# Kernel optimization log

Measured on AMD Instinct MI355X. Metric: run time of the kernel, lower is better.

Reference implementation:

```python
import jax, jax.numpy as jnp
import numpy as np

N_NODES = 100000
N_EDGES = 1600000
D_IN = 64
D_OUT = 64


def _sage_conv(x, Wl, b, Wr, src, dst, inv_deg):
    # mean-aggregate neighbor features: gather x[src], scatter-sum into dst, divide by degree
    agg = jax.ops.segment_sum(x[src], dst, num_segments=N_NODES)  # [N, d]
    agg = agg * inv_deg                                            # mean with deg clamped >= 1
    # PyG SAGEConv: lin_l(agg) (with bias) + lin_r(x) (no bias)
    return agg @ Wl.T + b + x @ Wr.T


def setup_inputs() -> dict:
    key = jax.random.key(0)
    ks = jax.random.split(key, 8)
    x = jax.random.normal(ks[0], (N_NODES, D_IN), dtype=jnp.float32)
    edge_index = jax.random.randint(ks[1], (2, N_EDGES), 0, N_NODES, dtype=jnp.int64)
    s1 = 1.0 / np.sqrt(D_IN)
    s2 = 1.0 / np.sqrt(D_OUT)
    Wl1 = jax.random.uniform(ks[2], (D_OUT, D_IN), jnp.float32, -s1, s1)
    b1 = jnp.zeros((D_OUT,), jnp.float32)
    Wr1 = jax.random.uniform(ks[3], (D_OUT, D_IN), jnp.float32, -s1, s1)
    Wl2 = jax.random.uniform(ks[4], (D_OUT, D_OUT), jnp.float32, -s2, s2)
    b2 = jnp.zeros((D_OUT,), jnp.float32)
    Wr2 = jax.random.uniform(ks[5], (D_OUT, D_OUT), jnp.float32, -s2, s2)
    return {"x": x, "edge_index": edge_index, "Wl1": Wl1, "b1": b1, "Wr1": Wr1,
            "Wl2": Wl2, "b2": b2, "Wr2": Wr2}


def reference(x, edge_index, Wl1, b1, Wr1, Wl2, b2, Wr2):
    src, dst = edge_index[0], edge_index[1]
    deg = jax.ops.segment_sum(jnp.ones((N_EDGES,), jnp.float32), dst, num_segments=N_NODES)
    inv_deg = (1.0 / jnp.maximum(deg, 1.0))[:, None]  # [N, 1]
    h = _sage_conv(x, Wl1, b1, Wr1, src, dst, inv_deg)
    h = _sage_conv(h, Wl2, b2, Wr2, src, dst, inv_deg)
    return h
```

## Files before the change

kernel.cpp:

```cpp
#include <hip/hip_runtime.h>
#include <hip/hip_bf16.h>

#define NN 100000
#define NE 1600000
#define NB 196
#define BCAP 9216
#define BIN_CHUNK 8192
#define BIN_BLKS ((NE + BIN_CHUNK - 1) / BIN_CHUNK)

typedef __attribute__((ext_vector_type(8))) short bf16x8;
typedef __attribute__((ext_vector_type(4))) float f32x4;

__device__ inline unsigned short f2bf(float f) {
    union { __hip_bfloat16 h; unsigned short u; } c;
    c.h = __float2bfloat16(f);
    return c.u;
}

__global__ __launch_bounds__(256) void k_prep(const float* __restrict__ x,
                                              unsigned short* __restrict__ xb,
                                              const float* __restrict__ Wl1,
                                              const float* __restrict__ Wr1,
                                              const float* __restrict__ Wl2,
                                              const float* __restrict__ Wr2,
                                              unsigned short* __restrict__ Wc1,
                                              unsigned short* __restrict__ Wc2,
                                              int* __restrict__ gcur) {
    int i = blockIdx.x * 256 + threadIdx.x;
    if (i < NB) gcur[i] = i * BCAP;
    if (i < 4096) {
        int fo = i >> 6, k = i & 63;
        Wc1[fo * 128 + k]      = f2bf(Wl1[i]);
        Wc1[fo * 128 + 64 + k] = f2bf(Wr1[i]);
        Wc2[fo * 128 + k]      = f2bf(Wl2[i]);
        Wc2[fo * 128 + 64 + k] = f2bf(Wr2[i]);
    }
    if (i < NN * 64 / 8) {
        const float4* p = (const float4*)(x + (size_t)i * 8);
        float4 v0 = p[0], v1 = p[1];
        union { bf16x8 v; unsigned short u[8]; } c;
        c.u[0] = f2bf(v0.x); c.u[1] = f2bf(v0.y); c.u[2] = f2bf(v0.z); c.u[3] = f2bf(v0.w);
        c.u[4] = f2bf(v1.x); c.u[5] = f2bf(v1.y); c.u[6] = f2bf(v1.z); c.u[7] = f2bf(v1.w);
        *(bf16x8*)(xb + (size_t)i * 8) = c.v;
    }
}

__global__ __launch_bounds__(256) void k_bin(const int* __restrict__ src,
                                             const int* __restrict__ dst,
                                             int* __restrict__ gcur,
                                             unsigned* __restrict__ binned) {
    __shared__ int hist[NB];
    __shared__ int base[NB];
    __shared__ int lcur[NB];
    const int t = threadIdx.x;
    const int e0 = blockIdx.x * BIN_CHUNK;
    const int n4 = min(BIN_CHUNK, NE - e0) >> 2;
    for (int i = t; i < NB; i += 256) { hist[i] = 0; lcur[i] = 0; }
    __syncthreads();
    const int4* d4p = (const int4*)(dst + e0);
    const int4* s4p = (const int4*)(src + e0);
    for (int i = t; i < n4; i += 256) {
        int4 d = d4p[i];
        atomicAdd(&hist[d.x >> 9], 1);
        atomicAdd(&hist[d.y >> 9], 1);
        atomicAdd(&hist[d.z >> 9], 1);
        atomicAdd(&hist[d.w >> 9], 1);
    }
    __syncthreads();
    for (int i = t; i < NB; i += 256) {
        int h = hist[i];
        base[i] = h ? atomicAdd(&gcur[i], h) : 0;
    }
    __syncthreads();
    for (int i = t; i < n4; i += 256) {
        int4 d = d4p[i];
        int4 s = s4p[i];
        #define PLACE(dd, ss) {                                         \
            int b = (dd) >> 9;                                          \
            int p = base[b] + atomicAdd(&lcur[b], 1);                   \
            binned[p] = ((unsigned)((dd) & 511) << 17) | (unsigned)(ss);}
        PLACE(d.x, s.x) PLACE(d.y, s.y) PLACE(d.z, s.z) PLACE(d.w, s.w)
        #undef PLACE
    }
}

__global__ __launch_bounds__(256) void k_csr(const int* __restrict__ gcur,
                                             unsigned* __restrict__ binned,
                                             int2* __restrict__ noff,
                                             float* __restrict__ inv) {
    __shared__ unsigned buf[BCAP];
    __shared__ int h[512];
    __shared__ int off[512];
    __shared__ int lcur[512];
    __shared__ int s[256];
    const int b = blockIdx.x;
    const int t = threadIdx.x;
    const int base = b * BCAP;
    const int cnt = min(gcur[b] - base, BCAP);
    for (int i = t; i < 512; i += 256) h[i] = 0;
    __syncthreads();
    for (int i = t; i < cnt; i += 256) {
        unsigned v = binned[base + i];
        buf[i] = v;
        atomicAdd(&h[v >> 17], 1);
    }
    __syncthreads();
    int a0 = h[2 * t], a1 = h[2 * t + 1];
    s[t] = a0 + a1;
    __syncthreads();
    #pragma unroll
    for (int o = 1; o < 256; o <<= 1) {
        int u = (t >= o) ? s[t - o] : 0;
        __syncthreads();
        s[t] += u;
        __syncthreads();
    }
    int ex = s[t] - (a0 + a1);
    off[2 * t] = ex;          lcur[2 * t] = ex;
    off[2 * t + 1] = ex + a0; lcur[2 * t + 1] = ex + a0;
    __syncthreads();
    for (int i = t; i < cnt; i += 256) {
        unsigned v = buf[i];
        int dl = v >> 17;
        int p = atomicAdd(&lcur[dl], 1);
        binned[base + p] = v & 0x1FFFFu;
    }
    #pragma unroll
    for (int q = 0; q < 2; ++q) {
        int l = 2 * t + q;
        int node = b * 512 + l;
        if (node < NN) {
            int st = base + off[l];
            noff[node] = make_int2(st, st + h[l]);
            inv[node] = 1.0f / fmaxf((float)h[l], 1.0f);
        }
    }
}

__global__ __launch_bounds__(512) void k_fused(const unsigned short* __restrict__ feat,
                                               const int2* __restrict__ noff,
                                               const unsigned* __restrict__ csr,
                                               const float* __restrict__ inv,
                                               const unsigned short* __restrict__ Wc,
                                               const float* __restrict__ bias,
                                               float* __restrict__ Cf,
                                               unsigned short* __restrict__ Cb) {
    __shared__ unsigned short sA[64 * 72];
    const int t = threadIdx.x;
    const int n0 = blockIdx.x * 64;

    {
        const int g = t >> 3;
        const int p = t & 7;
        const int node = n0 + g;
        float a[8] = {0.f, 0.f, 0.f, 0.f, 0.f, 0.f, 0.f, 0.f};
        float iv = 0.f;
        if (node < NN) {
            int2 oe = noff[node];
            int beg = oe.x, end = oe.y;
            iv = inv[node];

            #define UNPK(uu, k)                                        \
                a[2*(k)]   += __uint_as_float((uu) << 16);             \
                a[2*(k)+1] += __uint_as_float((uu) & 0xffff0000u);
            #define UNPK4(q0, q1, q2, q3)                              \
                UNPK(q0.x, 0) UNPK(q0.y, 1) UNPK(q0.z, 2) UNPK(q0.w, 3)\
                UNPK(q1.x, 0) UNPK(q1.y, 1) UNPK(q1.z, 2) UNPK(q1.w, 3)\
                UNPK(q2.x, 0) UNPK(q2.y, 1) UNPK(q2.z, 2) UNPK(q2.w, 3)\
                UNPK(q3.x, 0) UNPK(q3.y, 1) UNPK(q3.z, 2) UNPK(q3.w, 3)
            #define GATHER(s) (*(const uint4*)(feat + (size_t)(s) * 64 + p * 8))

            int j = beg;
            uint4 u0, u1, u2, u3;
            bool pending = false;
            if (j + 4 <= end) {
                u0 = GATHER(csr[j]);     u1 = GATHER(csr[j + 1]);
                u2 = GATHER(csr[j + 2]); u3 = GATHER(csr[j + 3]);
                j += 4;
                pending = true;
            }
            for (; j + 4 <= end; j += 4) {
                uint4 v0 = GATHER(csr[j]);     uint4 v1 = GATHER(csr[j + 1]);
                uint4 v2 = GATHER(csr[j + 2]); uint4 v3 = GATHER(csr[j + 3]);
                UNPK4(u0, u1, u2, u3)
                u0 = v0; u1 = v1; u2 = v2; u3 = v3;
            }
            if (pending) { UNPK4(u0, u1, u2, u3) }
            for (; j < end; ++j) {
                uint4 w0 = GATHER(csr[j]);
                UNPK(w0.x, 0) UNPK(w0.y, 1) UNPK(w0.z, 2) UNPK(w0.w, 3)
            }
            #undef GATHER
            #undef UNPK4
            #undef UNPK
        }
        union { bf16x8 v; unsigned short u[8]; } c;
        #pragma unroll
        for (int e = 0; e < 8; ++e) c.u[e] = f2bf(a[e] * iv);
        *(bf16x8*)(&sA[g * 72 + p * 8]) = c.v;
    }
    __syncthreads();

    const int w = t >> 6;
    const int l = t & 63;
    const int cn = l & 15;
    const int ks = l >> 4;
    const int s = w & 3;
    const int h = w >> 2;
    const int lrow = s * 16 + cn;
    const int arow = n0 + lrow;
    const int aclamp = (arow < NN) ? arow : 0;

    f32x4 acc0 = {0.f, 0.f, 0.f, 0.f};
    f32x4 acc1 = {0.f, 0.f, 0.f, 0.f};

    #pragma unroll
    for (int kb = 0; kb < 4; ++kb) {
        bf16x8 aa;
        if (kb < 2) aa = *(const bf16x8*)(&sA[lrow * 72 + kb * 32 + ks * 8]);
        else        aa = *(const bf16x8*)(feat + (size_t)aclamp * 64 + (kb - 2) * 32 + ks * 8);
        const unsigned short* wb = Wc + cn * 128 + kb * 32 + ks * 8;
        bf16x8 b0 = *(const bf16x8*)(wb + (size_t)(2 * h) * 16 * 128);
        bf16x8 b1 = *(const bf16x8*)(wb + (size_t)(2 * h + 1) * 16 * 128);
        acc0 = __builtin_amdgcn_mfma_f32_16x16x32_bf16(aa, b0, acc0, 0, 0, 0);
        acc1 = __builtin_amdgcn_mfma_f32_16x16x32_bf16(aa, b1, acc1, 0, 0, 0);
    }

    #pragma unroll
    for (int fb = 0; fb < 2; ++fb) {
        f32x4 av = fb ? acc1 : acc0;
        int f = 2 * h + fb;
        float bv = bias[f * 16 + cn];
        #pragma unroll
        for (int r = 0; r < 4; ++r) {
            int node = n0 + s * 16 + ks * 4 + r;
            if (node < NN) {
                float val = av[r] + bv;
                if (Cb) Cb[(size_t)node * 64 + f * 16 + cn] = f2bf(val);
                else    Cf[(size_t)node * 64 + f * 16 + cn] = val;
            }
        }
    }
}


extern "C" void kernel_launch(void* const* d_in, const int* in_sizes, int n_in,
                              void* d_out, int out_size, void* d_ws, size_t ws_size,
                              hipStream_t stream) {
    const float* x   = (const float*)d_in[0];
    const int*   ei  = (const int*)d_in[1];
    const int*   src = ei;
    const int*   dst = ei + NE;
    const float* Wl1 = (const float*)d_in[2];
    const float* b1  = (const float*)d_in[3];
    const float* Wr1 = (const float*)d_in[4];
    const float* Wl2 = (const float*)d_in[5];
    const float* b2  = (const float*)d_in[6];
    const float* Wr2 = (const float*)d_in[7];
    float* out = (float*)d_out;

    char* ws = (char*)d_ws;
    size_t off = 0;
    auto alloc = [&](size_t bytes) {
        void* p = ws + off;
        off = (off + bytes + 255) & ~(size_t)255;
        return p;
    };
    unsigned short* xb     = (unsigned short*)alloc(2 * (size_t)NN * 64);
    unsigned short* h1b    = (unsigned short*)alloc(2 * (size_t)NN * 64);
    unsigned*       binned = (unsigned*)alloc(sizeof(unsigned) * NB * BCAP);
    int2*           noff   = (int2*)alloc(sizeof(int2) * NN);
    float*          inv    = (float*)alloc(sizeof(float) * NN);
    int*            gcur   = (int*)alloc(sizeof(int) * NB);
    unsigned short* Wc1    = (unsigned short*)alloc(2 * 64 * 128);
    unsigned short* Wc2    = (unsigned short*)alloc(2 * 64 * 128);

    k_prep<<<(NN * 64 / 8 + 255) / 256, 256, 0, stream>>>(x, xb, Wl1, Wr1, Wl2, Wr2,
                                                          Wc1, Wc2, gcur);
    k_bin <<<BIN_BLKS, 256, 0, stream>>>(src, dst, gcur, binned);
    k_csr <<<NB, 256, 0, stream>>>(gcur, binned, noff, inv);

    k_fused<<<(NN + 63) / 64, 512, 0, stream>>>(xb, noff, binned, inv, Wc1, b1,
                                                (float*)nullptr, h1b);
    k_fused<<<(NN + 63) / 64, 512, 0, stream>>>(h1b, noff, binned, inv, Wc2, b2,
                                                out, (unsigned short*)nullptr);
}
```

Baseline: 140.7 us.

## Gather neighbor features in FP8 e4m3 instead of bf16 for aggregation

Adds FP8 (e4m3) copies of the input features and the layer-1 output, and the neighbor-gather aggregation now reads 8 bytes per lane instead of 16. This halves the bytes moved by the random-access gather, which dominates the fused kernels. The self term in the matmul still uses bf16. It also halves the binning chunk size to launch more bin blocks. The cost is extra FP8 writes in the prep and layer-1 epilogue, software FP8 encoding, and a real loss of accuracy in the aggregated features that may break tolerance.

```diff
diff --git a/kernel.cpp b/kernel.cpp
--- a/kernel.cpp
+++ b/kernel.cpp
@@ -5,7 +5,7 @@
 #define NE 1600000
 #define NB 196
 #define BCAP 9216
-#define BIN_CHUNK 8192
+#define BIN_CHUNK 4096
 #define BIN_BLKS ((NE + BIN_CHUNK - 1) / BIN_CHUNK)
 
 typedef __attribute__((ext_vector_type(8))) short bf16x8;
@@ -17,8 +17,35 @@
     return c.u;
 }
 
+__device__ inline unsigned f2e4m3(float f) {
+    unsigned u = __float_as_uint(f);
+    unsigned s = (u >> 24) & 0x80u;
+    unsigned b = u & 0x7FFFFFFFu;
+    float af = __uint_as_float(b);
+    if (af >= 464.f) return s | 0x7Eu;
+    if (af < 0.015625f) {
+        unsigned m = (unsigned)__float2int_rn(af * 512.f);
+        return s | m;
+    }
+    unsigned r = b + 0x7FFFFu + ((b >> 20) & 1u);
+    int e = (int)(r >> 23) - 127;
+    if (e > 8) return s | 0x7Eu;
+    return s | ((unsigned)(e + 7) << 3) | ((r >> 20) & 7u);
+}
+
+#if __has_builtin(__builtin_amdgcn_cvt_f32_fp8)
+#define FP8CVT(w, k) __builtin_amdgcn_cvt_f32_fp8((int)(w), (k))
+#else
+__device__ inline float fp8_manual(unsigned b) {
+    unsigned v = ((b & 0x80u) << 24) | ((b & 0x7Fu) << 20);
+    return __uint_as_float(v) * 0x1p120f;
+}
+#define FP8CVT(w, k) fp8_manual(((w) >> ((k) * 8)) & 0xFFu)
+#endif
+
 __global__ __launch_bounds__(256) void k_prep(const float* __restrict__ x,
                                               unsigned short* __restrict__ xb,
+                                              unsigned char* __restrict__ x8,
                                               const float* __restrict__ Wl1,
                                               const float* __restrict__ Wr1,
                                               const float* __restrict__ Wl2,
@@ -42,6 +69,11 @@
         c.u[0] = f2bf(v0.x); c.u[1] = f2bf(v0.y); c.u[2] = f2bf(v0.z); c.u[3] = f2bf(v0.w);
         c.u[4] = f2bf(v1.x); c.u[5] = f2bf(v1.y); c.u[6] = f2bf(v1.z); c.u[7] = f2bf(v1.w);
         *(bf16x8*)(xb + (size_t)i * 8) = c.v;
+        unsigned lo = f2e4m3(v0.x) | (f2e4m3(v0.y) << 8) |
+                      (f2e4m3(v0.z) << 16) | (f2e4m3(v0.w) << 24);
+        unsigned hi = f2e4m3(v1.x) | (f2e4m3(v1.y) << 8) |
+                      (f2e4m3(v1.z) << 16) | (f2e4m3(v1.w) << 24);
+        *(uint2*)(x8 + (size_t)i * 8) = make_uint2(lo, hi);
     }
 }
 
@@ -138,13 +170,15 @@
 }
 
 __global__ __launch_bounds__(512) void k_fused(const unsigned short* __restrict__ feat,
+                                               const unsigned char* __restrict__ f8,
                                                const int2* __restrict__ noff,
                                                const unsigned* __restrict__ csr,
                                                const float* __restrict__ inv,
                                                const unsigned short* __restrict__ Wc,
                                                const float* __restrict__ bias,
                                                float* __restrict__ Cf,
-                                               unsigned short* __restrict__ Cb) {
+                                               unsigned short* __restrict__ Cb,
+                                               unsigned char* __restrict__ C8) {
     __shared__ unsigned short sA[64 * 72];
     const int t = threadIdx.x;
     const int n0 = blockIdx.x * 64;
@@ -160,18 +194,15 @@
             int beg = oe.x, end = oe.y;
             iv = inv[node];
 
-            #define UNPK(uu, k)                                        \
-                a[2*(k)]   += __uint_as_float((uu) << 16);             \
-                a[2*(k)+1] += __uint_as_float((uu) & 0xffff0000u);
-            #define UNPK4(q0, q1, q2, q3)                              \
-                UNPK(q0.x, 0) UNPK(q0.y, 1) UNPK(q0.z, 2) UNPK(q0.w, 3)\
-                UNPK(q1.x, 0) UNPK(q1.y, 1) UNPK(q1.z, 2) UNPK(q1.w, 3)\
-                UNPK(q2.x, 0) UNPK(q2.y, 1) UNPK(q2.z, 2) UNPK(q2.w, 3)\
-                UNPK(q3.x, 0) UNPK(q3.y, 1) UNPK(q3.z, 2) UNPK(q3.w, 3)
-            #define GATHER(s) (*(const uint4*)(feat + (size_t)(s) * 64 + p * 8))
+            #define UNPK8(u)                                           \
+                a[0] += FP8CVT((u).x, 0); a[1] += FP8CVT((u).x, 1);    \
+                a[2] += FP8CVT((u).x, 2); a[3] += FP8CVT((u).x, 3);    \
+                a[4] += FP8CVT((u).y, 0); a[5] += FP8CVT((u).y, 1);    \
+                a[6] += FP8CVT((u).y, 2); a[7] += FP8CVT((u).y, 3);
+            #define GATHER(s) (*(const uint2*)(f8 + (size_t)(s) * 64 + p * 8))
 
             int j = beg;
-            uint4 u0, u1, u2, u3;
+            uint2 u0, u1, u2, u3;
             bool pending = false;
             if (j + 4 <= end) {
                 u0 = GATHER(csr[j]);     u1 = GATHER(csr[j + 1]);
@@ -180,19 +211,18 @@
                 pending = true;
             }
             for (; j + 4 <= end; j += 4) {
-                uint4 v0 = GATHER(csr[j]);     uint4 v1 = GATHER(csr[j + 1]);
-                uint4 v2 = GATHER(csr[j + 2]); uint4 v3 = GATHER(csr[j + 3]);
-                UNPK4(u0, u1, u2, u3)
+                uint2 v0 = GATHER(csr[j]);     uint2 v1 = GATHER(csr[j + 1]);
+                uint2 v2 = GATHER(csr[j + 2]); uint2 v3 = GATHER(csr[j + 3]);
+                UNPK8(u0) UNPK8(u1) UNPK8(u2) UNPK8(u3)
                 u0 = v0; u1 = v1; u2 = v2; u3 = v3;
             }
-            if (pending) { UNPK4(u0, u1, u2, u3) }
+            if (pending) { UNPK8(u0) UNPK8(u1) UNPK8(u2) UNPK8(u3) }
             for (; j < end; ++j) {
-                uint4 w0 = GATHER(csr[j]);
-                UNPK(w0.x, 0) UNPK(w0.y, 1) UNPK(w0.z, 2) UNPK(w0.w, 3)
+                uint2 w0 = GATHER(csr[j]);
+                UNPK8(w0)
             }
             #undef GATHER
-            #undef UNPK4
-            #undef UNPK
+            #undef UNPK8
         }
         union { bf16x8 v; unsigned short u[8]; } c;
         #pragma unroll
@@ -236,8 +266,12 @@
             int node = n0 + s * 16 + ks * 4 + r;
             if (node < NN) {
                 float val = av[r] + bv;
-                if (Cb) Cb[(size_t)node * 64 + f * 16 + cn] = f2bf(val);
-                else    Cf[(size_t)node * 64 + f * 16 + cn] = val;
+                if (Cb) {
+                    Cb[(size_t)node * 64 + f * 16 + cn] = f2bf(val);
+                    C8[(size_t)node * 64 + f * 16 + cn] = (unsigned char)f2e4m3(val);
+                } else {
+                    Cf[(size_t)node * 64 + f * 16 + cn] = val;
+                }
             }
         }
     }
@@ -268,6 +302,8 @@
     };
     unsigned short* xb     = (unsigned short*)alloc(2 * (size_t)NN * 64);
     unsigned short* h1b    = (unsigned short*)alloc(2 * (size_t)NN * 64);
+    unsigned char*  x8     = (unsigned char*)alloc((size_t)NN * 64);
+    unsigned char*  h18    = (unsigned char*)alloc((size_t)NN * 64);
     unsigned*       binned = (unsigned*)alloc(sizeof(unsigned) * NB * BCAP);
     int2*           noff   = (int2*)alloc(sizeof(int2) * NN);
     float*          inv    = (float*)alloc(sizeof(float) * NN);
@@ -275,13 +311,14 @@
     unsigned short* Wc1    = (unsigned short*)alloc(2 * 64 * 128);
     unsigned short* Wc2    = (unsigned short*)alloc(2 * 64 * 128);
 
-    k_prep<<<(NN * 64 / 8 + 255) / 256, 256, 0, stream>>>(x, xb, Wl1, Wr1, Wl2, Wr2,
+    k_prep<<<(NN * 64 / 8 + 255) / 256, 256, 0, stream>>>(x, xb, x8, Wl1, Wr1, Wl2, Wr2,
                                                           Wc1, Wc2, gcur);
     k_bin <<<BIN_BLKS, 256, 0, stream>>>(src, dst, gcur, binned);
     k_csr <<<NB, 256, 0, stream>>>(gcur, binned, noff, inv);
 
-    k_fused<<<(NN + 63) / 64, 512, 0, stream>>>(xb, noff, binned, inv, Wc1, b1,
-                                                (float*)nullptr, h1b);
-    k_fused<<<(NN + 63) / 64, 512, 0, stream>>>(h1b, noff, binned, inv, Wc2, b2,
-                                                out, (unsigned short*)nullptr);
-}
+    k_fused<<<(NN + 63) / 64, 512, 0, stream>>>(xb, x8, noff, binned, inv, Wc1, b1,
+                                                (float*)nullptr, h1b, h18);
+    k_fused<<<(NN + 63) / 64, 512, 0, stream>>>(h1b, h18, noff, binned, inv, Wc2, b2,
+                                                out, (unsigned short*)nullptr,
+                                                (unsigned char*)nullptr);
+}
```

Measured after the change: 141.1 us. Within noise of the previous version (+0.3%).
